# Kernel optimization log

Measured on AMD Instinct MI355X. Metric: run time of the kernel, lower is better.

## Reference

```python
import jax, jax.numpy as jnp
import numpy as np

ENC_DIM = 512
MEL_DIM = 80
PRENET = [128, 64]
DEC_DIM = 256
B, T_MEL, T_ENC = 64, 1000, 400


def setup_inputs() -> dict:
    key = jax.random.key(0)
    ks = jax.random.split(key, 20)
    s = 0.05
    inp = {
        "mel_input": jax.random.normal(ks[0], (B, T_MEL, MEL_DIM), jnp.float32),
        "encoder_outputs": jax.random.normal(ks[1], (B, T_ENC, ENC_DIM), jnp.float32),
        # Prenet: Linear(80->128), Linear(128->64)
        "W_p1": jax.random.normal(ks[2], (PRENET[0], MEL_DIM), jnp.float32) * s,
        "b_p1": jnp.zeros((PRENET[0],), jnp.float32),
        "W_p2": jax.random.normal(ks[3], (PRENET[1], PRENET[0]), jnp.float32) * s,
        "b_p2": jnp.zeros((PRENET[1],), jnp.float32),
        # Attention: query_layer Linear(dec->enc), energy Linear(enc->1)
        "W_q": jax.random.normal(ks[4], (ENC_DIM, DEC_DIM), jnp.float32) * s,
        "b_q": jnp.zeros((ENC_DIM,), jnp.float32),
        "W_e": jax.random.normal(ks[5], (1, ENC_DIM), jnp.float32) * s,
        "b_e": jnp.zeros((1,), jnp.float32),
        # LSTM: input = prenet_out(64) + context(512) = 576 -> hidden 256
        "W_ih": jax.random.normal(ks[6], (4 * DEC_DIM, PRENET[1] + ENC_DIM), jnp.float32) * s,
        "W_hh": jax.random.normal(ks[7], (4 * DEC_DIM, DEC_DIM), jnp.float32) * s,
        "b_ih": jnp.zeros((4 * DEC_DIM,), jnp.float32),
        "b_hh": jnp.zeros((4 * DEC_DIM,), jnp.float32),
        # Output projection Linear(256->80)
        "W_out": jax.random.normal(ks[8], (MEL_DIM, DEC_DIM), jnp.float32) * s,
        "b_out": jnp.zeros((MEL_DIM,), jnp.float32),
    }
    return inp


def _decoder(mel_input, encoder_outputs, W_p1, b_p1, W_p2, b_p2,
             W_q, b_q, W_e, b_e, W_ih, W_hh, b_ih, b_hh, W_out, b_out):
    # Prenet (dropout in eval mode / identity): [B, T_mel, 64]
    x = jax.nn.relu(jnp.einsum('btm,pm->btp', mel_input, W_p1) + b_p1)
    x = jax.nn.relu(jnp.einsum('btp,qp->btq', x, W_p2) + b_p2)

    h0 = jnp.zeros((mel_input.shape[0], DEC_DIM), mel_input.dtype)
    c0 = jnp.zeros_like(h0)
    w_e = W_e[0]  # [enc]
    b_e0 = b_e[0]

    def step(carry, x_t):
        h, c = carry
        # Bahdanau attention using previous hidden state as query
        q = h @ W_q.T + b_q                                   # [B, enc]
        energy = jnp.tanh(q[:, None, :] + encoder_outputs) @ w_e + b_e0  # [B, T_enc]
        attn = jax.nn.softmax(energy, axis=-1)
        context = jnp.einsum('bt,bte->be', attn, encoder_outputs)        # [B, enc]
        # LSTM cell (torch gate order i, f, g, o)
        lstm_in = jnp.concatenate([x_t, context], axis=-1)    # [B, 64+enc]
        gates = lstm_in @ W_ih.T + b_ih + h @ W_hh.T + b_hh   # [B, 4H]
        i, f, g, o = jnp.split(gates, 4, axis=-1)
        c_new = jax.nn.sigmoid(f) * c + jax.nn.sigmoid(i) * jnp.tanh(g)
        h_new = jax.nn.sigmoid(o) * jnp.tanh(c_new)
        mel_out = h_new @ W_out.T + b_out                     # [B, mel]
        return (h_new, c_new), mel_out

    _, outs = jax.lax.scan(step, (h0, c0), jnp.swapaxes(x, 0, 1))  # [T, B, mel]
    return jnp.swapaxes(outs, 0, 1)  # [B, T_mel, mel]


def reference(mel_input, encoder_outputs, W_p1, b_p1, W_p2, b_p2,
              W_q, b_q, W_e, b_e, W_ih, W_hh, b_ih, b_hh, W_out, b_out):
    return _decoder(mel_input, encoder_outputs, W_p1, b_p1, W_p2, b_p2,
                    W_q, b_q, W_e, b_e, W_ih, W_hh, b_ih, b_hh, W_out, b_out)
```

## Files before the change

kernel.cpp:

```cpp
#include <hip/hip_runtime.h>
#include <hip/hip_fp16.h>

#define NB     64
#define TMEL   1000
#define TE     400
#define ENC    512
#define MELD   80
#define P1     128
#define P2     64
#define HID    256
#define KCOMB  832

#define OFF_ENCH  0u
#define OFF_XH    26214400u
#define OFF_WCH   34406400u
#define OFF_WQS   36110336u
#define OFF_WOS   36372480u
#define OFF_BSQ   36413440u
#define OFF_WP1T  36417536u
#define OFF_WP2T  36458496u
#define OFF_COMM  36491264u
#define OFF_BAR   37801984u

#define SEG1 13107200
#define SEG2 851968
#define SEG3 131072
#define SEG4 20480
#define SEG5 1024
#define SEG6 10240
#define SEG7 8192
#define SEG8 4096
#define PREP_TOT (SEG1+SEG2+SEG3+SEG4+SEG5+SEG6+SEG7+SEG8)

#define L_ENC   0u
#define L_WOS   102400u
#define L_SCR   112640u
#define L_Q     145408u
#define L_LIN   147456u
#define L_EN    150784u
#define L_GATE  151296u
#define L_H     152320u
#define L_C     152576u
#define L_RED   152832u
#define SMEM_BYTES 152896

__device__ __forceinline__ float fast_tanh(float x) {
    float e = __expf(2.f * x);
    return 1.f - 2.f * __builtin_amdgcn_rcpf(e + 1.f);
}
__device__ __forceinline__ float fast_sigmoid(float x) {
    return __builtin_amdgcn_rcpf(1.f + __expf(-x));
}

__device__ __forceinline__ float gload(const float* p) {
    return __hip_atomic_load(p, __ATOMIC_RELAXED, __HIP_MEMORY_SCOPE_AGENT);
}
__device__ __forceinline__ void gstore(float* p, float v) {
    __hip_atomic_store(p, v, __ATOMIC_RELAXED, __HIP_MEMORY_SCOPE_AGENT);
}

__global__ void prep_kernel(const float* __restrict__ enc,
                            const float* __restrict__ Wq,
                            const float* __restrict__ Wih,
                            const float* __restrict__ Whh,
                            const float* __restrict__ Wout,
                            const float* __restrict__ Wp1,
                            const float* __restrict__ Wp2,
                            const float* __restrict__ bih,
                            const float* __restrict__ bhh,
                            char* __restrict__ wsb) {
    long i = (long)blockIdx.x * blockDim.x + threadIdx.x;
    if (i >= PREP_TOT) return;
    if (i < SEG1) {
        ((__half*)(wsb + OFF_ENCH))[i] = __float2half(enc[i]);
        return;
    }
    i -= SEG1;
    if (i < SEG2) {
        int m  = (int)(i / (KCOMB * 256));
        int rr = (int)(i % (KCOMB * 256));
        int k  = rr / 256, jj = rr % 256;
        int gate = jj >> 6, u = jj & 63;
        int jg = gate * 256 + m * 64 + u;
        float v = (k < 576) ? Wih[(size_t)jg * 576 + k] : Whh[(size_t)jg * 256 + (k - 576)];
        ((__half*)(wsb + OFF_WCH))[i] = __float2half(v);
        return;
    }
    i -= SEG2;
    if (i < SEG3) {
        int m = (int)(i / (64 * 512));
        int rr = (int)(i % (64 * 512));
        int kk = rr / 512, j = rr % 512;
        ((__half*)(wsb + OFF_WQS))[i] = __float2half(Wq[(size_t)j * 256 + m * 64 + kk]);
        return;
    }
    i -= SEG3;
    if (i < SEG4) {
        int m = (int)(i / (64 * 80));
        int rr = (int)(i % (64 * 80));
        int kk = rr / 80, jo = rr % 80;
        ((__half*)(wsb + OFF_WOS))[i] = __float2half(Wout[(size_t)jo * 256 + m * 64 + kk]);
        return;
    }
    i -= SEG4;
    if (i < SEG5) {
        int m = (int)(i / 256), jj = (int)(i % 256);
        int gate = jj >> 6, u = jj & 63;
        int jg = gate * 256 + m * 64 + u;
        ((float*)(wsb + OFF_BSQ))[i] = bih[jg] + bhh[jg];
        return;
    }
    i -= SEG5;
    if (i < SEG6) {
        int j = (int)(i & 127), k = (int)(i >> 7);
        ((float*)(wsb + OFF_WP1T))[i] = Wp1[j * 80 + k];
        return;
    }
    i -= SEG6;
    if (i < SEG7) {
        int j = (int)(i & 63), k = (int)(i >> 6);
        ((float*)(wsb + OFF_WP2T))[i] = Wp2[j * 128 + k];
        return;
    }
    i -= SEG7;
    ((int*)(wsb + OFF_BAR))[i] = 0;
}

__global__ __launch_bounds__(128) void prenet_kernel(const float* __restrict__ mel,
                                                     const float* __restrict__ bp1,
                                                     const float* __restrict__ bp2,
                                                     char* __restrict__ wsb) {
    __shared__ float mel_sh[MELD];
    __shared__ float hid_sh[P1];
    const float* wp1T = (const float*)(wsb + OFF_WP1T);
    const float* wp2T = (const float*)(wsb + OFF_WP2T);
    __half* xH = (__half*)(wsb + OFF_XH);
    int bt = blockIdx.x;
    int tid = threadIdx.x;
    if (tid < MELD) mel_sh[tid] = mel[(size_t)bt * MELD + tid];
    __syncthreads();
    {
        float acc = bp1[tid];
        #pragma unroll 4
        for (int k = 0; k < MELD; ++k) acc += mel_sh[k] * wp1T[k * P1 + tid];
        hid_sh[tid] = fmaxf(acc, 0.f);
    }
    __syncthreads();
    if (tid < P2) {
        float acc = bp2[tid];
        #pragma unroll 4
        for (int k = 0; k < P1; ++k) acc += hid_sh[k] * wp2T[k * P2 + tid];
        xH[(size_t)bt * P2 + tid] = __float2half(fmaxf(acc, 0.f));
    }
}

__device__ __forceinline__ void groupbar(int* c, int n) {
    __syncthreads();
    if (threadIdx.x == 0) {
        __hip_atomic_fetch_add(c, 1, __ATOMIC_RELAXED, __HIP_MEMORY_SCOPE_AGENT);
        while (__hip_atomic_load(c, __ATOMIC_RELAXED, __HIP_MEMORY_SCOPE_AGENT) < 4 * n)
            __builtin_amdgcn_s_sleep(1);
    }
    __syncthreads();
}

__global__ __launch_bounds__(1024, 1) void decoder_kernel(const float* __restrict__ bq,
                                                          const float* __restrict__ we,
                                                          const float* __restrict__ bout,
                                                          char* __restrict__ wsb,
                                                          float* __restrict__ out) {
    extern __shared__ __align__(16) char smem[];
    __half* encL     = (__half*)(smem + L_ENC);
    __half* wosL     = (__half*)(smem + L_WOS);
    float*  scr      = (float*)(smem + L_SCR);
    float*  q_sh     = (float*)(smem + L_Q);
    float*  lin_sh   = (float*)(smem + L_LIN);
    float*  en_sh    = (float*)(smem + L_EN);
    float*  gates_sh = (float*)(smem + L_GATE);
    float*  h_sh     = (float*)(smem + L_H);
    float*  c_sh     = (float*)(smem + L_C);
    float*  red_sh   = (float*)(smem + L_RED);

    const int bid  = blockIdx.x;
    const int g    = bid & 63;
    const int m    = bid >> 6;
    const int tid  = threadIdx.x;
    const int lane = tid & 63;
    const int wv   = tid >> 6;

    const __half* encH = (const __half*)(wsb + OFF_ENCH) + (size_t)g * TE * ENC + (size_t)m * 100 * ENC;
    const __half* xH   = (const __half*)(wsb + OFF_XH) + (size_t)g * TMEL * P2;
    const __half* wc   = (const __half*)(wsb + OFF_WCH) + (size_t)m * KCOMB * 256;
    const __half* wqs  = (const __half*)(wsb + OFF_WQS) + (size_t)m * 64 * 512;
    const __half* wos  = (const __half*)(wsb + OFF_WOS) + (size_t)m * 64 * 80;
    const float*  bsq  = (const float*)(wsb + OFF_BSQ) + m * 256;
    char*  comm = wsb + OFF_COMM + (size_t)g * 20480;
    float* qp   = (float*)(comm);
    float* ctxp = (float*)(comm + 8192);
    float* ml   = (float*)(comm + 16384);
    float* hq   = (float*)(comm + 16512);
    float* melp = (float*)(comm + 18560);
    int*   barc = (int*)(wsb + OFF_BAR) + g * 64;
    float* outB = out + (size_t)g * TMEL * MELD;

    {
        const int4* s1 = (const int4*)encH;
        int4* d1 = (int4*)encL;
        for (int i = tid; i < 6400; i += 1024) d1[i] = s1[i];
        const int4* s2 = (const int4*)wos;
        int4* d2 = (int4*)wosL;
        if (tid < 640) d2[tid] = s2[tid];
    }

    if (tid < 512) gstore(&qp[m * 512 + tid], 0.f);
    if (tid < 64) {
        gstore(&hq[m * 64 + tid], 0.f);
        gstore(&hq[256 + m * 64 + tid], 0.f);
        h_sh[tid] = 0.f;
        c_sh[tid] = 0.f;
    }
    groupbar(barc, 1);

    float4 wa = ((const float4*)we)[lane * 2];
    float4 wb = ((const float4*)we)[lane * 2 + 1];
    float wsum = wa.x + wa.y + wa.z + wa.w + wb.x + wb.y + wb.z + wb.w;
    wa.x *= 2.f; wa.y *= 2.f; wa.z *= 2.f; wa.w *= 2.f;
    wb.x *= 2.f; wb.y *= 2.f; wb.z *= 2.f; wb.w *= 2.f;
    const float C2 = 2.8853900817779268f;

    const float* wq2 = (const float*)wqs;

    for (int t = 0; t < TMEL; ++t) {
        if (m == 0 && t > 0 && tid < MELD) {
            float o = bout[tid] + gload(&melp[tid]) + gload(&melp[80 + tid]) +
                      gload(&melp[160 + tid]) + gload(&melp[240 + tid]);
            outB[(size_t)(t - 1) * MELD + tid] = o;
        }
        if (tid < ENC)
            q_sh[tid] = bq[tid] + gload(&qp[tid]) + gload(&qp[512 + tid]) +
                        gload(&qp[1024 + tid]) + gload(&qp[1536 + tid]);
        __syncthreads();

        {
            float4 qa = ((const float4*)q_sh)[lane * 2];
            float4 qb = ((const float4*)q_sh)[lane * 2 + 1];
            int r = wv;
            float4 raw = ((const float4*)(encL + (size_t)r * ENC))[lane];
            while (r < 100) {
                int rn = r + 16;
                int rc = (rn < 100) ? rn : 0;
                float4 rawn = ((const float4*)(encL + (size_t)rc * ENC))[lane];
                const __half2* hp = (const __half2*)&raw;
                float p = wsum;
                float2 e;
                #define ETERM(qv, w2v, ev) { float a_ = (qv) + (ev); \
                    float x_ = exp2f(a_ * C2); \
                    float r_ = __builtin_amdgcn_rcpf(x_ + 1.f); \
                    p = fmaf(-(w2v), r_, p); }
                e = __half22float2(hp[0]); ETERM(qa.x, wa.x, e.x); ETERM(qa.y, wa.y, e.y);
                e = __half22float2(hp[1]); ETERM(qa.z, wa.z, e.x); ETERM(qa.w, wa.w, e.y);
                e = __half22float2(hp[2]); ETERM(qb.x, wb.x, e.x); ETERM(qb.y, wb.y, e.y);
                e = __half22float2(hp[3]); ETERM(qb.z, wb.z, e.x); ETERM(qb.w, wb.w, e.y);
                #undef ETERM
                #pragma unroll
                for (int off = 32; off; off >>= 1) p += __shfl_xor(p, off, 64);
                if (lane == 0) en_sh[r] = p;
                raw = rawn; r = rn;
            }
        }
        __syncthreads();
        if (wv == 0) {
            float mx = (lane < 100) ? en_sh[lane] : -1e30f;
            if (lane < 36) mx = fmaxf(mx, en_sh[64 + lane]);
            #pragma unroll
            for (int off = 32; off; off >>= 1) mx = fmaxf(mx, __shfl_xor(mx, off, 64));
            if (lane == 0) red_sh[0] = mx;
        }
        __syncthreads();
        if (tid < 100) en_sh[tid] = __expf(en_sh[tid] - red_sh[0]);
        __syncthreads();
        if (wv == 0) {
            float s = (lane < 100) ? en_sh[lane] : 0.f;
            if (lane < 36) s += en_sh[64 + lane];
            #pragma unroll
            for (int off = 32; off; off >>= 1) s += __shfl_xor(s, off, 64);
            if (lane == 0) red_sh[1] = s;
        }
        {
            float4 a0 = {0.f, 0.f, 0.f, 0.f}, a1 = {0.f, 0.f, 0.f, 0.f};
            int r = wv;
            float4 raw = ((const float4*)(encL + (size_t)r * ENC))[lane];
            while (r < 100) {
                int rn = r + 16;
                int rc = (rn < 100) ? rn : 0;
                float4 rawn = ((const float4*)(encL + (size_t)rc * ENC))[lane];
                float ex = en_sh[r];
                const __half2* hp = (const __half2*)&raw;
                float2 e;
                e = __half22float2(hp[0]); a0.x = fmaf(ex, e.x, a0.x); a0.y = fmaf(ex, e.y, a0.y);
                e = __half22float2(hp[1]); a0.z = fmaf(ex, e.x, a0.z); a0.w = fmaf(ex, e.y, a0.w);
                e = __half22float2(hp[2]); a1.x = fmaf(ex, e.x, a1.x); a1.y = fmaf(ex, e.y, a1.y);
                e = __half22float2(hp[3]); a1.z = fmaf(ex, e.x, a1.z); a1.w = fmaf(ex, e.y, a1.w);
                raw = rawn; r = rn;
            }
            ((float4*)(scr + wv * 512))[lane * 2] = a0;
            ((float4*)(scr + wv * 512))[lane * 2 + 1] = a1;
        }
        __syncthreads();
        if (tid < ENC) {
            float c = 0.f;
            #pragma unroll
            for (int w = 0; w < 16; ++w) c += scr[w * 512 + tid];
            gstore(&ctxp[m * 512 + tid], c);
        }
        if (tid == 0) { gstore(&ml[m * 2], red_sh[0]); gstore(&ml[m * 2 + 1], red_sh[1]); }

        const int kb = wv * 52;
        const float2* wp = (const float2*)wc + (size_t)kb * 64 + lane;
        float2 wbuf[4][4];
        #pragma unroll
        for (int gg = 0; gg < 4; ++gg) {
            #pragma unroll
            for (int i = 0; i < 4; ++i) wbuf[gg][i] = wp[(size_t)(4 * gg + i) * 64];
        }

        groupbar(barc, 2 * t + 2);

        float c0, c1, c2, c3, xv, hv;
        if (tid < ENC) {
            c0 = gload(&ctxp[tid]);        c1 = gload(&ctxp[512 + tid]);
            c2 = gload(&ctxp[1024 + tid]); c3 = gload(&ctxp[1536 + tid]);
        }
        if (tid < P2) xv = __half2float(xH[(size_t)t * P2 + tid]);
        if (tid >= 512 && tid < 768) hv = gload(&hq[(t & 1) * 256 + (tid - 512)]);
        if (tid < 8) red_sh[4 + tid] = gload(&ml[tid]);
        __syncthreads();
        float M = fmaxf(fmaxf(red_sh[4], red_sh[6]), fmaxf(red_sh[8], red_sh[10]));
        float s0 = __expf(red_sh[4] - M), s1 = __expf(red_sh[6] - M);
        float s2 = __expf(red_sh[8] - M), s3 = __expf(red_sh[10] - M);
        float linv = __builtin_amdgcn_rcpf(s0 * red_sh[5] + s1 * red_sh[7] +
                                           s2 * red_sh[9] + s3 * red_sh[11]);
        if (tid < ENC) lin_sh[64 + tid] = (s0 * c0 + s1 * c1 + s2 * c2 + s3 * c3) * linv;
        if (tid < P2) lin_sh[tid] = xv;
        if (tid >= 512 && tid < 768) lin_sh[576 + (tid - 512)] = hv;
        __syncthreads();

        {
            float4 acc = {0.f, 0.f, 0.f, 0.f};
            #pragma unroll
            for (int gg = 0; gg < 13; ++gg) {
                float2 w0 = wbuf[gg & 3][0], w1 = wbuf[gg & 3][1];
                float2 w2 = wbuf[gg & 3][2], w3 = wbuf[gg & 3][3];
                if (gg + 4 < 13) {
                    #pragma unroll
                    for (int i = 0; i < 4; ++i)
                        wbuf[gg & 3][i] = wp[(size_t)(4 * (gg + 4) + i) * 64];
                }
                {
                    float s = lin_sh[kb + 4 * gg + 0];
                    const __half2* hp = (const __half2*)&w0;
                    float2 wA = __half22float2(hp[0]), wB = __half22float2(hp[1]);
                    acc.x = fmaf(s, wA.x, acc.x); acc.y = fmaf(s, wA.y, acc.y);
                    acc.z = fmaf(s, wB.x, acc.z); acc.w = fmaf(s, wB.y, acc.w);
                }
                {
                    float s = lin_sh[kb + 4 * gg + 1];
                    const __half2* hp = (const __half2*)&w1;
                    float2 wA = __half22float2(hp[0]), wB = __half22float2(hp[1]);
                    acc.x = fmaf(s, wA.x, acc.x); acc.y = fmaf(s, wA.y, acc.y);
                    acc.z = fmaf(s, wB.x, acc.z); acc.w = fmaf(s, wB.y, acc.w);
                }
                {
                    float s = lin_sh[kb + 4 * gg + 2];
                    const __half2* hp = (const __half2*)&w2;
                    float2 wA = __half22float2(hp[0]), wB = __half22float2(hp[1]);
                    acc.x = fmaf(s, wA.x, acc.x); acc.y = fmaf(s, wA.y, acc.y);
                    acc.z = fmaf(s, wB.x, acc.z); acc.w = fmaf(s, wB.y, acc.w);
                }
                {
                    float s = lin_sh[kb + 4 * gg + 3];
                    const __half2* hp = (const __half2*)&w3;
                    float2 wA = __half22float2(hp[0]), wB = __half22float2(hp[1]);
                    acc.x = fmaf(s, wA.x, acc.x); acc.y = fmaf(s, wA.y, acc.y);
                    acc.z = fmaf(s, wB.x, acc.z); acc.w = fmaf(s, wB.y, acc.w);
                }
            }
            ((float4*)(scr + wv * 256))[lane] = acc;
        }

        float qbuf[2][16];
        if (tid < 256) {
            #pragma unroll
            for (int gg = 0; gg < 2; ++gg) {
                #pragma unroll
                for (int i = 0; i < 16; ++i)
                    qbuf[gg][i] = wq2[(size_t)(16 * gg + i) * 256 + tid];
            }
        }
        __syncthreads();
        if (tid < 256) {
            float gsum = bsq[tid];
            #pragma unroll
            for (int w = 0; w < 16; ++w) gsum += scr[w * 256 + tid];
            gates_sh[tid] = gsum;
        }
        __syncthreads();
        if (tid < 64) {
            float ig = fast_sigmoid(gates_sh[tid]);
            float fg = fast_sigmoid(gates_sh[64 + tid]);
            float gg = fast_tanh(gates_sh[128 + tid]);
            float og = fast_sigmoid(gates_sh[192 + tid]);
            float cN = fmaf(fg, c_sh[tid], ig * gg);
            float hN = og * fast_tanh(cN);
            c_sh[tid] = cN; h_sh[tid] = hN;
            gstore(&hq[((t + 1) & 1) * 256 + m * 64 + tid], hN);
        }
        __syncthreads();
        if (tid < 256) {
            float a0 = 0.f, a1 = 0.f;
            #pragma unroll
            for (int gg = 0; gg < 4; ++gg) {
                float rr[16];
                #pragma unroll
                for (int i = 0; i < 16; ++i) rr[i] = qbuf[gg & 1][i];
                if (gg + 2 < 4) {
                    #pragma unroll
                    for (int i = 0; i < 16; ++i)
                        qbuf[gg & 1][i] = wq2[(size_t)(16 * (gg + 2) + i) * 256 + tid];
                }
                #pragma unroll
                for (int i = 0; i < 16; ++i) {
                    __half2 hh = *(const __half2*)&rr[i];
                    float2 w = __half22float2(hh);
                    float h = h_sh[16 * gg + i];
                    a0 = fmaf(h, w.x, a0); a1 = fmaf(h, w.y, a1);
                }
            }
            gstore(&qp[m * 512 + 2 * tid], a0);
            gstore(&qp[m * 512 + 2 * tid + 1], a1);
        }
        if (tid >= 512 && tid < 512 + MELD) {
            int jo = tid - 512;
            float a = 0.f;
            #pragma unroll 8
            for (int kk = 0; kk < 64; ++kk) a = fmaf(h_sh[kk], __half2float(wosL[kk * 80 + jo]), a);
            gstore(&melp[m * 80 + jo], a);
        }
        groupbar(barc, 2 * t + 3);
    }
    if (m == 0 && tid < MELD) {
        float o = bout[tid] + gload(&melp[tid]) + gload(&melp[80 + tid]) +
                  gload(&melp[160 + tid]) + gload(&melp[240 + tid]);
        outB[(size_t)(TMEL - 1) * MELD + tid] = o;
    }
}

extern "C" void kernel_launch(void* const* d_in, const int* in_sizes, int n_in,
                              void* d_out, int out_size, void* d_ws, size_t ws_size,
                              hipStream_t stream) {
    (void)in_sizes; (void)n_in; (void)out_size; (void)ws_size;
    const float* mel  = (const float*)d_in[0];
    const float* enc  = (const float*)d_in[1];
    const float* Wp1  = (const float*)d_in[2];
    const float* bp1  = (const float*)d_in[3];
    const float* Wp2  = (const float*)d_in[4];
    const float* bp2  = (const float*)d_in[5];
    const float* Wq   = (const float*)d_in[6];
    const float* bq   = (const float*)d_in[7];
    const float* We   = (const float*)d_in[8];
    const float* Wih  = (const float*)d_in[10];
    const float* Whh  = (const float*)d_in[11];
    const float* bih  = (const float*)d_in[12];
    const float* bhh  = (const float*)d_in[13];
    const float* Wout = (const float*)d_in[14];
    const float* bout = (const float*)d_in[15];
    char* wsb  = (char*)d_ws;
    float* out = (float*)d_out;

    long prepBlocks = (PREP_TOT + 255) / 256;
    prep_kernel<<<dim3((unsigned)prepBlocks), 256, 0, stream>>>(
        enc, Wq, Wih, Whh, Wout, Wp1, Wp2, bih, bhh, wsb);
    prenet_kernel<<<NB * TMEL, 128, 0, stream>>>(mel, bp1, bp2, wsb);

    hipFuncSetAttribute((const void*)decoder_kernel,
                        hipFuncAttributeMaxDynamicSharedMemorySize, SMEM_BYTES);

    const float* bq_a = bq; const float* we_a = We; const float* bo_a = bout;
    char* ws_a = wsb; float* out_a = out;
    void* args[] = { &bq_a, &we_a, &bo_a, &ws_a, &out_a };
    hipLaunchCooperativeKernel((const void*)decoder_kernel, dim3(256), dim3(1024),
                               args, SMEM_BYTES, stream);
}
```

Measured before the change: 49.03 ms.

## Fold tanh scale into prepped weights, fuse softmax reductions, widen gate-matvec loads

Pre-multiplies the fp16 encoder copy and Wq by the 2/ln2 constant so the attention energy loop skips one multiply per element, and compensates by scaling the context by its inverse. Replaces the separate max and sum reduction passes, with their extra block barriers, by per-wave running max and sum written to shared memory. Restructures the LSTM gate matvec to load 8 halfs per lane as float4 with two k-parities per wave, combined by a cross-half shuffle. Hoists the x and h loads ahead of the step so their latency overlaps the attention work. Scaling the fp16 encoder values risks extra rounding error, and the new weight indexing must match the existing layout.

After: 44.77 ms. -8.7%, faster.

```diff
diff --git a/kernel.cpp b/kernel.cpp
--- a/kernel.cpp
+++ b/kernel.cpp
@@ -10,6 +10,9 @@
 #define P2     64
 #define HID    256
 #define KCOMB  832
+
+#define C2F    2.8853900817779268f
+#define INVC2F 0.34657359027997264f
 
 #define OFF_ENCH  0u
 #define OFF_XH    26214400u
@@ -72,7 +75,7 @@
     long i = (long)blockIdx.x * blockDim.x + threadIdx.x;
     if (i >= PREP_TOT) return;
     if (i < SEG1) {
-        ((__half*)(wsb + OFF_ENCH))[i] = __float2half(enc[i]);
+        ((__half*)(wsb + OFF_ENCH))[i] = __float2half(enc[i] * C2F);
         return;
     }
     i -= SEG1;
@@ -91,7 +94,7 @@
         int m = (int)(i / (64 * 512));
         int rr = (int)(i % (64 * 512));
         int kk = rr / 512, j = rr % 512;
-        ((__half*)(wsb + OFF_WQS))[i] = __float2half(Wq[(size_t)j * 256 + m * 64 + kk]);
+        ((__half*)(wsb + OFF_WQS))[i] = __float2half(Wq[(size_t)j * 256 + m * 64 + kk] * C2F);
         return;
     }
     i -= SEG3;
@@ -226,24 +229,33 @@
     float wsum = wa.x + wa.y + wa.z + wa.w + wb.x + wb.y + wb.z + wb.w;
     wa.x *= 2.f; wa.y *= 2.f; wa.z *= 2.f; wa.w *= 2.f;
     wb.x *= 2.f; wb.y *= 2.f; wb.z *= 2.f; wb.w *= 2.f;
-    const float C2 = 2.8853900817779268f;
 
     const float* wq2 = (const float*)wqs;
 
+    const int kb   = wv * 52;
+    const int jb   = (lane & 31) * 8;
+    const int kpar = lane >> 5;
+    const float4* wp4 = (const float4*)(wc + (size_t)(kb + kpar) * 256) + (lane & 31);
+
     for (int t = 0; t < TMEL; ++t) {
+        float xv = 0.f, hv = 0.f;
+        if (tid < P2) xv = __half2float(xH[(size_t)t * P2 + tid]);
+        if (tid >= 512 && tid < 768) hv = gload(&hq[(t & 1) * 256 + (tid - 512)]);
+
         if (m == 0 && t > 0 && tid < MELD) {
             float o = bout[tid] + gload(&melp[tid]) + gload(&melp[80 + tid]) +
                       gload(&melp[160 + tid]) + gload(&melp[240 + tid]);
             outB[(size_t)(t - 1) * MELD + tid] = o;
         }
         if (tid < ENC)
-            q_sh[tid] = bq[tid] + gload(&qp[tid]) + gload(&qp[512 + tid]) +
-                        gload(&qp[1024 + tid]) + gload(&qp[1536 + tid]);
+            q_sh[tid] = fmaf(bq[tid], C2F, gload(&qp[tid]) + gload(&qp[512 + tid]) +
+                                           gload(&qp[1024 + tid]) + gload(&qp[1536 + tid]));
         __syncthreads();
 
         {
             float4 qa = ((const float4*)q_sh)[lane * 2];
             float4 qb = ((const float4*)q_sh)[lane * 2 + 1];
+            float mx = -1e30f;
             int r = wv;
             float4 raw = ((const float4*)(encL + (size_t)r * ENC))[lane];
             while (r < 100) {
@@ -253,8 +265,7 @@
                 const __half2* hp = (const __half2*)&raw;
                 float p = wsum;
                 float2 e;
-                #define ETERM(qv, w2v, ev) { float a_ = (qv) + (ev); \
-                    float x_ = exp2f(a_ * C2); \
+                #define ETERM(qv_, w2v, ev) { float x_ = exp2f((qv_) + (ev)); \
                     float r_ = __builtin_amdgcn_rcpf(x_ + 1.f); \
                     p = fmaf(-(w2v), r_, p); }
                 e = __half22float2(hp[0]); ETERM(qa.x, wa.x, e.x); ETERM(qa.y, wa.y, e.y);
@@ -264,30 +275,24 @@
                 #undef ETERM
                 #pragma unroll
                 for (int off = 32; off; off >>= 1) p += __shfl_xor(p, off, 64);
+                mx = fmaxf(mx, p);
                 if (lane == 0) en_sh[r] = p;
                 raw = rawn; r = rn;
             }
-        }
-        __syncthreads();
-        if (wv == 0) {
-            float mx = (lane < 100) ? en_sh[lane] : -1e30f;
-            if (lane < 36) mx = fmaxf(mx, en_sh[64 + lane]);
-            #pragma unroll
-            for (int off = 32; off; off >>= 1) mx = fmaxf(mx, __shfl_xor(mx, off, 64));
-            if (lane == 0) red_sh[0] = mx;
-        }
-        __syncthreads();
-        if (tid < 100) en_sh[tid] = __expf(en_sh[tid] - red_sh[0]);
-        __syncthreads();
-        if (wv == 0) {
-            float s = (lane < 100) ? en_sh[lane] : 0.f;
-            if (lane < 36) s += en_sh[64 + lane];
-            #pragma unroll
-            for (int off = 32; off; off >>= 1) s += __shfl_xor(s, off, 64);
-            if (lane == 0) red_sh[1] = s;
-        }
+            if (lane == 0) gates_sh[32 + wv] = mx;
+        }
+        __syncthreads();
+        if (tid < 100) {
+            float M = gates_sh[32];
+            #pragma unroll
+            for (int w = 1; w < 16; ++w) M = fmaxf(M, gates_sh[32 + w]);
+            if (tid == 0) red_sh[0] = M;
+            en_sh[tid] = __expf(en_sh[tid] - M);
+        }
+        __syncthreads();
         {
             float4 a0 = {0.f, 0.f, 0.f, 0.f}, a1 = {0.f, 0.f, 0.f, 0.f};
+            float ssum = 0.f;
             int r = wv;
             float4 raw = ((const float4*)(encL + (size_t)r * ENC))[lane];
             while (r < 100) {
@@ -295,6 +300,7 @@
                 int rc = (rn < 100) ? rn : 0;
                 float4 rawn = ((const float4*)(encL + (size_t)rc * ENC))[lane];
                 float ex = en_sh[r];
+                ssum += ex;
                 const __half2* hp = (const __half2*)&raw;
                 float2 e;
                 e = __half22float2(hp[0]); a0.x = fmaf(ex, e.x, a0.x); a0.y = fmaf(ex, e.y, a0.y);
@@ -305,6 +311,7 @@
             }
             ((float4*)(scr + wv * 512))[lane * 2] = a0;
             ((float4*)(scr + wv * 512))[lane * 2 + 1] = a1;
+            if (lane == 0) gates_sh[wv] = ssum;
         }
         __syncthreads();
         if (tid < ENC) {
@@ -313,79 +320,64 @@
             for (int w = 0; w < 16; ++w) c += scr[w * 512 + tid];
             gstore(&ctxp[m * 512 + tid], c);
         }
-        if (tid == 0) { gstore(&ml[m * 2], red_sh[0]); gstore(&ml[m * 2 + 1], red_sh[1]); }
-
-        const int kb = wv * 52;
-        const float2* wp = (const float2*)wc + (size_t)kb * 64 + lane;
-        float2 wbuf[4][4];
+        if (tid == 0) {
+            float S = gates_sh[0];
+            #pragma unroll
+            for (int w = 1; w < 16; ++w) S += gates_sh[w];
+            gstore(&ml[m * 2], red_sh[0]);
+            gstore(&ml[m * 2 + 1], S);
+        }
+
+        float4 wbuf[4];
         #pragma unroll
-        for (int gg = 0; gg < 4; ++gg) {
-            #pragma unroll
-            for (int i = 0; i < 4; ++i) wbuf[gg][i] = wp[(size_t)(4 * gg + i) * 64];
-        }
+        for (int gg = 0; gg < 4; ++gg) wbuf[gg] = wp4[(size_t)gg * 64];
 
         groupbar(barc, 2 * t + 2);
 
-        float c0, c1, c2, c3, xv, hv;
+        float c0 = 0.f, c1 = 0.f, c2 = 0.f, c3 = 0.f;
         if (tid < ENC) {
             c0 = gload(&ctxp[tid]);        c1 = gload(&ctxp[512 + tid]);
             c2 = gload(&ctxp[1024 + tid]); c3 = gload(&ctxp[1536 + tid]);
         }
-        if (tid < P2) xv = __half2float(xH[(size_t)t * P2 + tid]);
-        if (tid >= 512 && tid < 768) hv = gload(&hq[(t & 1) * 256 + (tid - 512)]);
         if (tid < 8) red_sh[4 + tid] = gload(&ml[tid]);
         __syncthreads();
         float M = fmaxf(fmaxf(red_sh[4], red_sh[6]), fmaxf(red_sh[8], red_sh[10]));
         float s0 = __expf(red_sh[4] - M), s1 = __expf(red_sh[6] - M);
         float s2 = __expf(red_sh[8] - M), s3 = __expf(red_sh[10] - M);
         float linv = __builtin_amdgcn_rcpf(s0 * red_sh[5] + s1 * red_sh[7] +
-                                           s2 * red_sh[9] + s3 * red_sh[11]);
+                                           s2 * red_sh[9] + s3 * red_sh[11]) * INVC2F;
         if (tid < ENC) lin_sh[64 + tid] = (s0 * c0 + s1 * c1 + s2 * c2 + s3 * c3) * linv;
         if (tid < P2) lin_sh[tid] = xv;
         if (tid >= 512 && tid < 768) lin_sh[576 + (tid - 512)] = hv;
         __syncthreads();
 
         {
-            float4 acc = {0.f, 0.f, 0.f, 0.f};
-            #pragma unroll
-            for (int gg = 0; gg < 13; ++gg) {
-                float2 w0 = wbuf[gg & 3][0], w1 = wbuf[gg & 3][1];
-                float2 w2 = wbuf[gg & 3][2], w3 = wbuf[gg & 3][3];
-                if (gg + 4 < 13) {
-                    #pragma unroll
-                    for (int i = 0; i < 4; ++i)
-                        wbuf[gg & 3][i] = wp[(size_t)(4 * (gg + 4) + i) * 64];
-                }
-                {
-                    float s = lin_sh[kb + 4 * gg + 0];
-                    const __half2* hp = (const __half2*)&w0;
-                    float2 wA = __half22float2(hp[0]), wB = __half22float2(hp[1]);
-                    acc.x = fmaf(s, wA.x, acc.x); acc.y = fmaf(s, wA.y, acc.y);
-                    acc.z = fmaf(s, wB.x, acc.z); acc.w = fmaf(s, wB.y, acc.w);
-                }
-                {
-                    float s = lin_sh[kb + 4 * gg + 1];
-                    const __half2* hp = (const __half2*)&w1;
-                    float2 wA = __half22float2(hp[0]), wB = __half22float2(hp[1]);
-                    acc.x = fmaf(s, wA.x, acc.x); acc.y = fmaf(s, wA.y, acc.y);
-                    acc.z = fmaf(s, wB.x, acc.z); acc.w = fmaf(s, wB.y, acc.w);
-                }
-                {
-                    float s = lin_sh[kb + 4 * gg + 2];
-                    const __half2* hp = (const __half2*)&w2;
-                    float2 wA = __half22float2(hp[0]), wB = __half22float2(hp[1]);
-                    acc.x = fmaf(s, wA.x, acc.x); acc.y = fmaf(s, wA.y, acc.y);
-                    acc.z = fmaf(s, wB.x, acc.z); acc.w = fmaf(s, wB.y, acc.w);
-                }
-                {
-                    float s = lin_sh[kb + 4 * gg + 3];
-                    const __half2* hp = (const __half2*)&w3;
-                    float2 wA = __half22float2(hp[0]), wB = __half22float2(hp[1]);
-                    acc.x = fmaf(s, wA.x, acc.x); acc.y = fmaf(s, wA.y, acc.y);
-                    acc.z = fmaf(s, wB.x, acc.z); acc.w = fmaf(s, wB.y, acc.w);
-                }
-            }
-            ((float4*)(scr + wv * 256))[lane] = acc;
+            float a0 = 0.f, a1 = 0.f, a2 = 0.f, a3 = 0.f;
+            float a4 = 0.f, a5 = 0.f, a6 = 0.f, a7 = 0.f;
+            #pragma unroll
+            for (int gg = 0; gg < 26; ++gg) {
+                float4 w = wbuf[gg & 3];
+                if (gg + 4 < 26) wbuf[gg & 3] = wp4[(size_t)(gg + 4) * 64];
+                float s = lin_sh[kb + 2 * gg + kpar];
+                const __half2* hp = (const __half2*)&w;
+                float2 w01 = __half22float2(hp[0]), w23 = __half22float2(hp[1]);
+                float2 w45 = __half22float2(hp[2]), w67 = __half22float2(hp[3]);
+                a0 = fmaf(s, w01.x, a0); a1 = fmaf(s, w01.y, a1);
+                a2 = fmaf(s, w23.x, a2); a3 = fmaf(s, w23.y, a3);
+                a4 = fmaf(s, w45.x, a4); a5 = fmaf(s, w45.y, a5);
+                a6 = fmaf(s, w67.x, a6); a7 = fmaf(s, w67.y, a7);
+            }
+            a0 += __shfl_xor(a0, 32, 64); a1 += __shfl_xor(a1, 32, 64);
+            a2 += __shfl_xor(a2, 32, 64); a3 += __shfl_xor(a3, 32, 64);
+            a4 += __shfl_xor(a4, 32, 64); a5 += __shfl_xor(a5, 32, 64);
+            a6 += __shfl_xor(a6, 32, 64); a7 += __shfl_xor(a7, 32, 64);
+            if (lane < 32) {
+                float4 lo = {a0, a1, a2, a3};
+                float4 hi = {a4, a5, a6, a7};
+                float4* dst = (float4*)(scr + wv * 256 + jb);
+                dst[0] = lo;
+                dst[1] = hi;
+            }
         }
 
         float qbuf[2][16];
```
